# Kernel tuning notes

Measured on AMD Instinct MI355X. Metric: run time of the kernel, lower is better.

## Reference

```python
import jax, jax.numpy as jnp
import numpy as np

BS, SEQ, DIM = 4, 2048, 1024
N_EXPERTS = 8


def setup_inputs() -> dict:
    key = jax.random.key(0)
    k_x, k_w, k_i = jax.random.split(key, 3)
    X = jax.random.normal(k_x, (BS, SEQ, DIM), dtype=jnp.float32)
    # trunc_normal init with std = in_features ** -0.5 (plain normal is fine for a reference)
    W = jax.random.normal(k_w, (N_EXPERTS, DIM, DIM), dtype=jnp.float32) * (DIM ** -0.5)
    indices = jax.random.randint(k_i, (BS, SEQ), 0, N_EXPERTS, dtype=jnp.int32)
    return {"X": X, "W": W, "indices": indices}


def reference(X, W, indices):
    # Y[b, s, :] = X[b, s, :] @ W[indices[b, s]].T   (F.linear semantics)
    # Dense per-expert matmuls + masked accumulate: avoids gathering a
    # [bs, seq, out, in] weight tensor; loop is over the small fixed expert count.
    n = W.shape[0]
    Y = jnp.zeros(X.shape[:2] + (W.shape[1],), dtype=X.dtype)
    for e in range(n):
        mask = (indices == e)[..., None]                      # [bs, seq, 1]
        Ye = jnp.einsum('bsd,od->bso', X, W[e])               # [bs, seq, out]
        Y = jnp.where(mask, Ye, Y)
    return Y
```

## Files before the change

kernel.cpp:

```cpp
#include <hip/hip_runtime.h>
#include <stdint.h>

#define T_TOK 8192
#define DIMK 1024
#define NEXP 8
#define BM 128
#define BN 128
#define BK 64
#define NTK (DIMK / BK)
#define MAXROWS (T_TOK + NEXP * BM)
#define MAXTILES (T_TOK / BM + NEXP)
#define NT (DIMK / BN)
#define NWG (MAXTILES * NT)

typedef __attribute__((ext_vector_type(4))) float f32x4;
typedef __attribute__((ext_vector_type(8))) short short8;
typedef __attribute__((ext_vector_type(8))) unsigned short us8;

__device__ __forceinline__ unsigned short f2bf(float f) {
  uint32_t u = __builtin_bit_cast(uint32_t, f);
  u += 0x7FFFu + ((u >> 16) & 1u);
  return (unsigned short)(u >> 16);
}

__device__ __forceinline__ void gload_lds16(const void* g, void* l) {
  __builtin_amdgcn_global_load_lds(
      (const __attribute__((address_space(1))) void*)g,
      (__attribute__((address_space(3))) void*)l, 16, 0, 0);
}

__global__ void k_prep_conv(const int* __restrict__ idx, const float* __restrict__ W,
                            const float* __restrict__ X, int* __restrict__ hdr,
                            int* __restrict__ row2tok, unsigned short* __restrict__ Wb,
                            unsigned short* __restrict__ Xb) {
  const int tid = threadIdx.x;
  const int b = blockIdx.x;
  if (b == 0) {
    __shared__ int h[NEXP];
    __shared__ int cur[NEXP];
    __shared__ int segs[NEXP + 1];
    if (tid < NEXP) h[tid] = 0;
    __syncthreads();
    for (int i = tid; i < T_TOK; i += 256) atomicAdd(&h[idx[i]], 1);
    __syncthreads();
    if (tid == 0) {
      int off = 0;
      for (int e = 0; e < NEXP; e++) {
        segs[e] = off; cur[e] = off;
        hdr[e] = h[e]; hdr[8 + e] = off;
        off += ((h[e] + BM - 1) >> 7) << 7;
      }
      segs[NEXP] = off;
    }
    __syncthreads();
    for (int e = 0; e < NEXP; e++)
      for (int p = segs[e] + h[e] + tid; p < segs[e + 1]; p += 256) row2tok[p] = -1;
    for (int p = segs[NEXP] + tid; p < MAXROWS; p += 256) row2tok[p] = -1;
    for (int i = tid; i < T_TOK; i += 256) {
      int e = idx[i];
      int pos = atomicAdd(&cur[e], 1);
      row2tok[pos] = i;
    }
    return;
  }
  const float* src;
  unsigned short* dst;
  if (b <= 4096) {
    size_t base = (size_t)(b - 1) * 2048 + tid * 8;
    src = W + base; dst = Wb + base;
  } else {
    size_t base = (size_t)(b - 4097) * 2048 + tid * 8;
    src = X + base; dst = Xb + base;
  }
  f32x4 v0 = *(const f32x4*)src;
  f32x4 v1 = *(const f32x4*)(src + 4);
  us8 o;
  o[0] = f2bf(v0[0]); o[1] = f2bf(v0[1]); o[2] = f2bf(v0[2]); o[3] = f2bf(v0[3]);
  o[4] = f2bf(v1[0]); o[5] = f2bf(v1[1]); o[6] = f2bf(v1[2]); o[7] = f2bf(v1[3]);
  *(us8*)dst = o;
}

__global__ __launch_bounds__(512, 6) void k_gemm(
    const unsigned short* __restrict__ Xb, const unsigned short* __restrict__ Wb,
    const int* __restrict__ hdr, const int* __restrict__ row2tok,
    float* __restrict__ out) {
  __shared__ unsigned short A_lds[BM * BK];
  __shared__ unsigned short B_lds[BN * BK];

  const int orig = blockIdx.x;
  const int wgid = (orig & 7) * (NWG / 8) + (orig >> 3);
  int tile = wgid >> 3;
  const int n0 = (wgid & 7) * BN;

  int e = -1, row0 = 0;
  for (int i = 0; i < NEXP; i++) {
    int te = (hdr[i] + BM - 1) >> 7;
    if (e < 0) {
      if (tile < te) { e = i; row0 = hdr[8 + i] + tile * BM; }
      else tile -= te;
    }
  }
  if (e < 0) return;

  const int tid = threadIdx.x;
  const int lane = tid & 63;
  const int wid = tid >> 6;
  const int wr = wid >> 2, wc = wid & 3;

  const int st_r = lane >> 3;
  const int st_cb = ((lane & 7) ^ st_r) << 4;

  const char* a_lane_base[2];
#pragma unroll
  for (int j = 0; j < 2; j++) {
    int r = (wid * 2 + j) * 8 + st_r;
    int tok = row2tok[row0 + r];
    if (tok < 0) tok = 0;
    a_lane_base[j] = (const char*)Xb + (size_t)tok * (DIMK * 2) + st_cb;
  }
  const char* b_base = (const char*)Wb + ((size_t)e * DIMK * DIMK + (size_t)n0 * DIMK) * 2;

  f32x4 acc[4][2];
  const f32x4 fzero = {0.f, 0.f, 0.f, 0.f};
#pragma unroll
  for (int m = 0; m < 4; m++)
#pragma unroll
    for (int n = 0; n < 2; n++) acc[m][n] = fzero;

  const int rsel = lane & 15;
  const int swz_r = (lane & 7) << 4;
  const int kgrp = (lane >> 4) << 4;

  int a_row_b[4], b_row_b[2];
#pragma unroll
  for (int m = 0; m < 4; m++) a_row_b[m] = (wr * 64 + m * 16 + rsel) * (BK * 2);
#pragma unroll
  for (int n = 0; n < 2; n++) b_row_b[n] = (wc * 32 + n * 16 + rsel) * (BK * 2);

  for (int kt = 0; kt < NTK; kt++) {
    const int k0b = kt * (BK * 2);
#pragma unroll
    for (int j = 0; j < 2; j++) {
      int c = wid * 2 + j;
      int r = c * 8 + st_r;
      gload_lds16(a_lane_base[j] + k0b, (char*)A_lds + c * 1024);
      gload_lds16(b_base + (size_t)r * (DIMK * 2) + k0b + st_cb, (char*)B_lds + c * 1024);
    }
    __syncthreads();
#pragma unroll
    for (int ks = 0; ks < 2; ks++) {
      const int kb = ks * 64 + kgrp;
      short8 av[4], bv[2];
#pragma unroll
      for (int m = 0; m < 4; m++)
        av[m] = *(const short8*)((const char*)A_lds + a_row_b[m] + (kb ^ swz_r));
#pragma unroll
      for (int n = 0; n < 2; n++)
        bv[n] = *(const short8*)((const char*)B_lds + b_row_b[n] + (kb ^ swz_r));
#pragma unroll
      for (int m = 0; m < 4; m++)
#pragma unroll
        for (int n = 0; n < 2; n++)
          acc[m][n] = __builtin_amdgcn_mfma_f32_16x16x32_bf16(av[m], bv[n], acc[m][n], 0, 0, 0);
    }
    __syncthreads();
  }

  const int rg4 = (lane >> 4) * 4;
#pragma unroll
  for (int m = 0; m < 4; m++) {
#pragma unroll
    for (int i = 0; i < 4; i++) {
      int rg = row0 + wr * 64 + m * 16 + rg4 + i;
      int tok = row2tok[rg];
      if (tok >= 0) {
        float* po = out + (size_t)tok * DIMK + n0 + wc * 32 + rsel;
#pragma unroll
        for (int n = 0; n < 2; n++) po[n * 16] = acc[m][n][i];
      }
    }
  }
}

extern "C" void kernel_launch(void* const* d_in, const int* in_sizes, int n_in,
                              void* d_out, int out_size, void* d_ws, size_t ws_size,
                              hipStream_t stream) {
  const float* X = (const float*)d_in[0];
  const float* W = (const float*)d_in[1];
  const int* idx = (const int*)d_in[2];
  float* out = (float*)d_out;
  char* ws = (char*)d_ws;

  int* hdr = (int*)ws;
  int* row2tok = (int*)(ws + 256);
  unsigned short* Wb = (unsigned short*)(ws + 65536);
  unsigned short* Xb = (unsigned short*)(ws + 65536 + 16777216);

  k_prep_conv<<<8193, 256, 0, stream>>>(idx, W, X, hdr, row2tok, Wb, Xb);
  k_gemm<<<NWG, 512, 0, stream>>>(Xb, Wb, hdr, row2tok, out);
}
```

Before: 60.61 us.

## Map expert tiles to XCDs so each expert's weights stay in one L2

Replaces the linear workgroup-to-tile mapping with an XCD-aware schedule. Each XCD (blockIdx & 7) takes up to nine row tiles of the expert with the same index across all eight N columns, and the overflow tiles of all experts are spread over the remaining slots. The aim is for each expert's weight matrix and its token rows to be reused within one XCD's L2 instead of being fetched by every XCD. The mapping is more complex, and load balance across XCDs depends on the expert histogram, which can leave some XCDs doing more work than others.

Result: no change. 59.73 us (-1.4%).

```diff
diff --git a/kernel.cpp b/kernel.cpp
--- a/kernel.cpp
+++ b/kernel.cpp
@@ -87,20 +87,33 @@
   __shared__ unsigned short A_lds[BM * BK];
   __shared__ unsigned short B_lds[BN * BK];
 
+  int T[NEXP];
+#pragma unroll
+  for (int i = 0; i < NEXP; i++) T[i] = (hdr[i] + BM - 1) >> 7;
+
   const int orig = blockIdx.x;
-  const int wgid = (orig & 7) * (NWG / 8) + (orig >> 3);
-  int tile = wgid >> 3;
-  const int n0 = (wgid & 7) * BN;
-
-  int e = -1, row0 = 0;
-  for (int i = 0; i < NEXP; i++) {
-    int te = (hdr[i] + BM - 1) >> 7;
-    if (e < 0) {
-      if (tile < te) { e = i; row0 = hdr[8 + i] + tile * BM; }
-      else tile -= te;
+  const int xcd = orig & 7;
+  const int slot = orig >> 3;
+  int e = -1, tl = 0, nq = 0;
+  {
+    int P = T[xcd] < 9 ? T[xcd] : 9;
+    if (slot < 8 * P) {
+      e = xcd; tl = slot % P; nq = slot / P;
+    } else {
+      int r = slot - 8 * P;
+      for (int i = 0; i < xcd; i++) r += 72 - 8 * (T[i] < 9 ? T[i] : 9);
+      for (int i = 0; i < NEXP && e < 0; i++) {
+        int ot = T[i] - 9;
+        if (ot > 0) {
+          if (r < 8 * ot) { e = i; tl = 9 + r % ot; nq = r / ot; }
+          else r -= 8 * ot;
+        }
+      }
     }
   }
   if (e < 0) return;
+  const int n0 = nq * BN;
+  const int row0 = hdr[8 + e] + tl * BM;
 
   const int tid = threadIdx.x;
   const int lane = tid & 63;
```
